# Kernel tuning notes

Hardware: AMD Instinct MI355X
Metric: run time of the kernel (lower is better)

The kernel has to match this reference:

```python
import jax, jax.numpy as jnp
import numpy as np

T, E, H = 65536, 512, 512  # seq_len, embedding_size, hidden_size (kernel_size=2)


def setup_inputs() -> dict:
    key = jax.random.key(0)
    k1, k2 = jax.random.split(key)
    x = jax.random.normal(k1, (T, E), dtype=jnp.float32)
    # nn.Linear(2*E, 3*H): weight [3H, 2E], bias [3H]. Store transposed for x @ W.
    W = jax.random.normal(k2, (2 * E, 3 * H), dtype=jnp.float32) * 0.02
    b = jnp.zeros((3 * H,), dtype=jnp.float32)
    return {"input": x, "W": W, "b": b}


def reference(input, W, b):
    x = input
    t, e = x.shape
    h_dim = W.shape[1] // 3
    # Shift input by one step (zero-padded) and concat: conv over kernel_size=2 window.
    x_prev = jnp.concatenate([jnp.zeros((1, e), x.dtype), x[:-1]], axis=0)  # [T, E]
    gates = jnp.concatenate([x, x_prev], axis=1) @ W + b  # [T, 3H]
    z = jnp.tanh(gates[:, :h_dim])                # cell candidate
    f = jax.nn.sigmoid(gates[:, h_dim:2 * h_dim])  # forget gate
    o = jax.nn.sigmoid(gates[:, 2 * h_dim:])       # output gate

    # fo-pool recurrence: c_t = f_t * c_{t-1} + (1 - f_t) * z_t ; h_t = o_t * c_t
    def step(c, zfo):
        z_t, f_t, o_t = zfo
        c_new = f_t * c + (1.0 - f_t) * z_t
        return c_new, (c_new, o_t * c_new)

    c0 = jnp.zeros((h_dim,), x.dtype)
    _, (cells, hiddens) = jax.lax.scan(step, c0, (z, f, o))
    # Match torch: (hidden_temp [T,H], h [1,H], c [1,H])
    return hiddens, hiddens[-1:], cells[-1:]
```

## Files before the change

kernel.cpp:

```cpp
#include <hip/hip_runtime.h>


#define T_LEN 65536
#define H3    1536
#define LC    64
#define NCHUNK 1024

typedef float f32x4 __attribute__((ext_vector_type(4)));
typedef short bf16x8 __attribute__((ext_vector_type(8)));

__device__ __forceinline__ unsigned short f2bf(float f) {
    unsigned int x = __builtin_bit_cast(unsigned int, f);
    x += 0x7fffu + ((x >> 16) & 1u);
    return (unsigned short)(x >> 16);
}
__device__ __forceinline__ float bf2f(unsigned short u) {
    return __builtin_bit_cast(float, ((unsigned int)u) << 16);
}
__device__ __forceinline__ float fsig(float x)  { return 1.f / (1.f + __expf(-x)); }
__device__ __forceinline__ float ftanh(float x) { return 2.f / (1.f + __expf(-2.f * x)) - 1.f; }

__device__ __forceinline__ void gload_lds16(const void* g, void* l) {
    __builtin_amdgcn_global_load_lds((const __attribute__((address_space(1))) void*)g,
                                     (__attribute__((address_space(3))) void*)l, 16, 0, 0);
}

__global__ void prep_x(const float* __restrict__ x, unsigned short* __restrict__ xp) {
    const long long nq = (512LL + (long long)T_LEN * 512) / 4;
    for (long long q = (long long)blockIdx.x * blockDim.x + threadIdx.x; q < nq;
         q += (long long)gridDim.x * blockDim.x) {
        ushort4 u;
        if (q < 128) {
            u.x = 0; u.y = 0; u.z = 0; u.w = 0;
        } else {
            const float4 v = *reinterpret_cast<const float4*>(x + q * 4 - 512);
            u.x = f2bf(v.x); u.y = f2bf(v.y); u.z = f2bf(v.z); u.w = f2bf(v.w);
        }
        *reinterpret_cast<ushort4*>(xp + q * 4) = u;
    }
}

__global__ void prep_w(const float* __restrict__ W, unsigned short* __restrict__ Wt) {
    const int n_el = 1024 * H3;
    for (int i = blockIdx.x * blockDim.x + threadIdx.x; i < n_el;
         i += gridDim.x * blockDim.x) {
        const int k = i / H3, n = i - k * H3;
        Wt[n * 1024 + k] = f2bf(W[i]);
    }
}

__global__ __launch_bounds__(256) void gemm_gates(
    const unsigned short* __restrict__ xp,
    const unsigned short* __restrict__ Wt,
    const float* __restrict__ bias,
    unsigned short* __restrict__ zfo)
{
    __shared__ unsigned short Alds[2][128 * 32];
    __shared__ unsigned short Blds[2][128 * 32];

    const int tid  = threadIdx.x;
    const int lane = tid & 63;
    const int w    = tid >> 6;
    const int wr   = w >> 1, wc = w & 1;

    const int flat = blockIdx.y * gridDim.x + blockIdx.x;
    const int idx  = (flat & 7) * 768 + (flat >> 3);
    const int nb   = (idx % 12) * 128;
    const long long t0 = (long long)(idx / 12) * 128;

    const int srow_l = lane >> 2;
    const int scol   = (((lane & 3) ^ ((lane >> 3) & 3)) * 8);

    auto stage = [&](int bb, int kt) {
        const int kb = kt * 32;
        const long long abase = (kb < 512) ? (long long)(512 + kb) : (long long)(kb - 512);
        #pragma unroll
        for (int j = 0; j < 2; ++j) {
            const int row = j * 64 + w * 16 + srow_l;
            gload_lds16(xp + abase + (t0 + row) * 512 + scol,
                        &Alds[bb][(j * 64 + w * 16) * 32]);
            gload_lds16(Wt + (long long)(nb + row) * 1024 + kb + scol,
                        &Blds[bb][(j * 64 + w * 16) * 32]);
        }
    };

    const int arow  = lane & 15;
    const int swzco = (((lane >> 4) ^ ((arow >> 1) & 3)) * 8);

    f32x4 acc[4][4] = {};

    stage(0, 0);
    asm volatile("s_waitcnt vmcnt(0)" ::: "memory");
    __syncthreads();

    for (int kt = 0; kt < 32; ++kt) {
        const int bb = kt & 1;
        if (kt + 1 < 32) stage(bb ^ 1, kt + 1);

        bf16x8 af[4], bfr[4];
        #pragma unroll
        for (int m = 0; m < 4; ++m)
            af[m] = *reinterpret_cast<const bf16x8*>(&Alds[bb][(wr * 64 + m * 16 + arow) * 32 + swzco]);
        #pragma unroll
        for (int n = 0; n < 4; ++n)
            bfr[n] = *reinterpret_cast<const bf16x8*>(&Blds[bb][(wc * 64 + n * 16 + arow) * 32 + swzco]);
        #pragma unroll
        for (int m = 0; m < 4; ++m)
            #pragma unroll
            for (int n = 0; n < 4; ++n)
                acc[m][n] = __builtin_amdgcn_mfma_f32_16x16x32_bf16(af[m], bfr[n], acc[m][n], 0, 0, 0);

        if (kt + 1 < 32) { asm volatile("s_waitcnt vmcnt(0)" ::: "memory"); }
        __syncthreads();
    }

    const int cls = nb >> 9;
    float bn[4];
    #pragma unroll
    for (int n = 0; n < 4; ++n) bn[n] = bias[nb + wc * 64 + n * 16 + arow];
    #pragma unroll
    for (int m = 0; m < 4; ++m) {
        #pragma unroll
        for (int n = 0; n < 4; ++n) {
            const int col = nb + wc * 64 + n * 16 + arow;
            #pragma unroll
            for (int j = 0; j < 4; ++j) {
                const long long row = t0 + wr * 64 + m * 16 + (lane >> 4) * 4 + j;
                float v = acc[m][n][j] + bn[n];
                v = (cls == 0) ? ftanh(v) : fsig(v);
                zfo[row * H3 + col] = f2bf(v);
            }
        }
    }
}

__global__ void scan_pass1(const unsigned short* __restrict__ zfo,
                           float* __restrict__ P, float* __restrict__ L) {
    const int chunk = blockIdx.x;
    const int c4    = threadIdx.x;
    const unsigned short* base = zfo + (long long)chunk * LC * H3 + c4 * 4;
    float c[4] = {0.f, 0.f, 0.f, 0.f};
    float p[4] = {1.f, 1.f, 1.f, 1.f};
    for (int t = 0; t < LC; ++t) {
        const unsigned short* row = base + t * H3;
        const ushort4 uz = *reinterpret_cast<const ushort4*>(row);
        const ushort4 uf = *reinterpret_cast<const ushort4*>(row + 512);
        const float z[4] = {bf2f(uz.x), bf2f(uz.y), bf2f(uz.z), bf2f(uz.w)};
        const float f[4] = {bf2f(uf.x), bf2f(uf.y), bf2f(uf.z), bf2f(uf.w)};
        #pragma unroll
        for (int j = 0; j < 4; ++j) {
            c[j] = fmaf(f[j], c[j] - z[j], z[j]);
            p[j] *= f[j];
        }
    }
    #pragma unroll
    for (int j = 0; j < 4; ++j) {
        P[chunk * 512 + c4 * 4 + j] = p[j];
        L[chunk * 512 + c4 * 4 + j] = c[j];
    }
}

__global__ __launch_bounds__(1024) void scan_pass2(
    const float* __restrict__ P, const float* __restrict__ L,
    float* __restrict__ carry, float* __restrict__ out) {
    const int ch = blockIdx.x;
    const int k  = threadIdx.x;
    __shared__ float sP[1024], sL[1024];
    float p = P[k * 512 + ch];
    float l = L[k * 512 + ch];
    sP[k] = p; sL[k] = l;
    __syncthreads();
    for (int d = 1; d < 1024; d <<= 1) {
        float pp = 1.f, ll = 0.f;
        if (k >= d) { pp = sP[k - d]; ll = sL[k - d]; }
        __syncthreads();
        l = fmaf(p, ll, l);
        p = p * pp;
        sP[k] = p; sL[k] = l;
        __syncthreads();
    }
    carry[k * 512 + ch] = (k == 0) ? 0.f : sL[k - 1];
    if (k == 1023) out[(long long)T_LEN * 512 + 512 + ch] = l;
}

__global__ void scan_pass3(const unsigned short* __restrict__ zfo,
                           const float* __restrict__ carry,
                           float* __restrict__ out) {
    const int chunk = blockIdx.x;
    const int c4    = threadIdx.x;
    const unsigned short* base = zfo + (long long)chunk * LC * H3 + c4 * 4;
    float c[4], h[4] = {0.f, 0.f, 0.f, 0.f};
    #pragma unroll
    for (int j = 0; j < 4; ++j) c[j] = carry[chunk * 512 + c4 * 4 + j];
    float4* outp = reinterpret_cast<float4*>(out + (long long)chunk * LC * 512) + c4;
    for (int t = 0; t < LC; ++t) {
        const unsigned short* row = base + t * H3;
        const ushort4 uz = *reinterpret_cast<const ushort4*>(row);
        const ushort4 uf = *reinterpret_cast<const ushort4*>(row + 512);
        const ushort4 uo = *reinterpret_cast<const ushort4*>(row + 1024);
        const float z[4] = {bf2f(uz.x), bf2f(uz.y), bf2f(uz.z), bf2f(uz.w)};
        const float f[4] = {bf2f(uf.x), bf2f(uf.y), bf2f(uf.z), bf2f(uf.w)};
        const float o[4] = {bf2f(uo.x), bf2f(uo.y), bf2f(uo.z), bf2f(uo.w)};
        #pragma unroll
        for (int j = 0; j < 4; ++j) {
            c[j] = fmaf(f[j], c[j] - z[j], z[j]);
            h[j] = o[j] * c[j];
        }
        float4 hv; hv.x = h[0]; hv.y = h[1]; hv.z = h[2]; hv.w = h[3];
        outp[t * 128] = hv;
    }
    if (chunk == NCHUNK - 1) {
        #pragma unroll
        for (int j = 0; j < 4; ++j)
            out[(long long)T_LEN * 512 + c4 * 4 + j] = h[j];
    }
}

extern "C" void kernel_launch(void* const* d_in, const int* in_sizes, int n_in,
                              void* d_out, int out_size, void* d_ws, size_t ws_size,
                              hipStream_t stream) {
    const float* x = (const float*)d_in[0];
    const float* W = (const float*)d_in[1];
    const float* b = (const float*)d_in[2];
    float* out = (float*)d_out;

    char* ws = (char*)d_ws;
    unsigned short* xp  = (unsigned short*)(ws);
    unsigned short* Wt  = (unsigned short*)(ws + 67110912LL);
    unsigned short* zfo = (unsigned short*)(ws + 70256640LL);
    float* P     = (float*)(ws);
    float* L     = (float*)(ws + 4194304LL);
    float* carry = (float*)(ws + 8388608LL);

    prep_x<<<4096, 256, 0, stream>>>(x, xp);
    prep_w<<<768, 256, 0, stream>>>(W, Wt);

    dim3 gg(H3 / 128, T_LEN / 128, 1);
    gemm_gates<<<gg, 256, 0, stream>>>(xp, Wt, b, zfo);

    scan_pass1<<<NCHUNK, 128, 0, stream>>>(zfo, P, L);
    scan_pass2<<<512, 1024, 0, stream>>>(P, L, carry, out);
    scan_pass3<<<NCHUNK, 128, 0, stream>>>(zfo, carry, out);
}
```

Measured before the change: 442.3 us.

## Triple-buffer GEMM LDS staging with partial waitcnt and faster activations

Moves the gates GEMM from double to triple buffering of LDS tiles. Each step waits only for the older loads (vmcnt(4)) and uses a raw s_barrier, so the next tile's global-to-LDS loads overlap the MFMA work. Global pointers are now advanced incrementally, with a jump where the A source switches from the current row to the shifted row. The activations use the hardware exp2 and rcp intrinsics, and launch bounds request 3 blocks per CU. This costs more LDS and risks register or occupancy limits, plus lower accuracy in the approximate sigmoid and tanh.

Result: faster. 393.7 us (-11.0%).

```diff
diff --git a/kernel.cpp b/kernel.cpp
--- a/kernel.cpp
+++ b/kernel.cpp
@@ -17,8 +17,12 @@
 __device__ __forceinline__ float bf2f(unsigned short u) {
     return __builtin_bit_cast(float, ((unsigned int)u) << 16);
 }
-__device__ __forceinline__ float fsig(float x)  { return 1.f / (1.f + __expf(-x)); }
-__device__ __forceinline__ float ftanh(float x) { return 2.f / (1.f + __expf(-2.f * x)) - 1.f; }
+__device__ __forceinline__ float fsig(float x) {
+    return __builtin_amdgcn_rcpf(1.f + __builtin_amdgcn_exp2f(-1.44269504f * x));
+}
+__device__ __forceinline__ float ftanh(float x) {
+    return 2.f * __builtin_amdgcn_rcpf(1.f + __builtin_amdgcn_exp2f(-2.88539008f * x)) - 1.f;
+}
 
 __device__ __forceinline__ void gload_lds16(const void* g, void* l) {
     __builtin_amdgcn_global_load_lds((const __attribute__((address_space(1))) void*)g,
@@ -49,14 +53,14 @@
     }
 }
 
-__global__ __launch_bounds__(256) void gemm_gates(
+__global__ __launch_bounds__(256, 3) void gemm_gates(
     const unsigned short* __restrict__ xp,
     const unsigned short* __restrict__ Wt,
     const float* __restrict__ bias,
     unsigned short* __restrict__ zfo)
 {
-    __shared__ unsigned short Alds[2][128 * 32];
-    __shared__ unsigned short Blds[2][128 * 32];
+    __shared__ unsigned short Alds[3][128 * 32];
+    __shared__ unsigned short Blds[3][128 * 32];
 
     const int tid  = threadIdx.x;
     const int lane = tid & 63;
@@ -71,17 +75,14 @@
     const int srow_l = lane >> 2;
     const int scol   = (((lane & 3) ^ ((lane >> 3) & 3)) * 8);
 
-    auto stage = [&](int bb, int kt) {
-        const int kb = kt * 32;
-        const long long abase = (kb < 512) ? (long long)(512 + kb) : (long long)(kb - 512);
-        #pragma unroll
-        for (int j = 0; j < 2; ++j) {
-            const int row = j * 64 + w * 16 + srow_l;
-            gload_lds16(xp + abase + (t0 + row) * 512 + scol,
-                        &Alds[bb][(j * 64 + w * 16) * 32]);
-            gload_lds16(Wt + (long long)(nb + row) * 1024 + kb + scol,
-                        &Blds[bb][(j * 64 + w * 16) * 32]);
-        }
+    const unsigned short* gA = xp + (t0 + w * 16 + srow_l) * 512 + 512 + scol;
+    const unsigned short* gB = Wt + (long long)(nb + w * 16 + srow_l) * 1024 + scol;
+
+    auto stage = [&](unsigned short* Al, unsigned short* Bl) {
+        gload_lds16(gA,             Al + (w * 16) * 32);
+        gload_lds16(gA + 64 * 512,  Al + ((64 + w * 16)) * 32);
+        gload_lds16(gB,             Bl + (w * 16) * 32);
+        gload_lds16(gB + 64 * 1024, Bl + ((64 + w * 16)) * 32);
     };
 
     const int arow  = lane & 15;
@@ -89,30 +90,53 @@
 
     f32x4 acc[4][4] = {};
 
-    stage(0, 0);
-    asm volatile("s_waitcnt vmcnt(0)" ::: "memory");
-    __syncthreads();
-
-    for (int kt = 0; kt < 32; ++kt) {
-        const int bb = kt & 1;
-        if (kt + 1 < 32) stage(bb ^ 1, kt + 1);
-
+    auto compute = [&](const unsigned short* Al, const unsigned short* Bl) {
         bf16x8 af[4], bfr[4];
         #pragma unroll
         for (int m = 0; m < 4; ++m)
-            af[m] = *reinterpret_cast<const bf16x8*>(&Alds[bb][(wr * 64 + m * 16 + arow) * 32 + swzco]);
+            af[m] = *reinterpret_cast<const bf16x8*>(Al + (wr * 64 + m * 16 + arow) * 32 + swzco);
         #pragma unroll
         for (int n = 0; n < 4; ++n)
-            bfr[n] = *reinterpret_cast<const bf16x8*>(&Blds[bb][(wc * 64 + n * 16 + arow) * 32 + swzco]);
+            bfr[n] = *reinterpret_cast<const bf16x8*>(Bl + (wc * 64 + n * 16 + arow) * 32 + swzco);
         #pragma unroll
         for (int m = 0; m < 4; ++m)
             #pragma unroll
             for (int n = 0; n < 4; ++n)
                 acc[m][n] = __builtin_amdgcn_mfma_f32_16x16x32_bf16(af[m], bfr[n], acc[m][n], 0, 0, 0);
-
-        if (kt + 1 < 32) { asm volatile("s_waitcnt vmcnt(0)" ::: "memory"); }
-        __syncthreads();
-    }
+    };
+
+    stage(Alds[0], Blds[0]); gA += 32; gB += 32;
+    stage(Alds[1], Blds[1]); gA += 32; gB += 32;
+    asm volatile("s_waitcnt vmcnt(4)" ::: "memory");
+    __builtin_amdgcn_s_barrier();
+
+    for (int kt = 0; kt < 30; kt += 3) {
+        {
+            stage(Alds[2], Blds[2]);
+            gA += (kt + 2 == 15) ? -992 : 32;  gB += 32;
+            compute(Alds[0], Blds[0]);
+            asm volatile("s_waitcnt vmcnt(4)" ::: "memory");
+            __builtin_amdgcn_s_barrier();
+        }
+        {
+            stage(Alds[0], Blds[0]);
+            gA += (kt + 3 == 15) ? -992 : 32;  gB += 32;
+            compute(Alds[1], Blds[1]);
+            asm volatile("s_waitcnt vmcnt(4)" ::: "memory");
+            __builtin_amdgcn_s_barrier();
+        }
+        {
+            stage(Alds[1], Blds[1]);
+            gA += (kt + 4 == 15) ? -992 : 32;  gB += 32;
+            compute(Alds[2], Blds[2]);
+            asm volatile("s_waitcnt vmcnt(4)" ::: "memory");
+            __builtin_amdgcn_s_barrier();
+        }
+    }
+    compute(Alds[0], Blds[0]);
+    asm volatile("s_waitcnt vmcnt(0)" ::: "memory");
+    __builtin_amdgcn_s_barrier();
+    compute(Alds[1], Blds[1]);
 
     const int cls = nb >> 9;
     float bn[4];
```

## Rewrite gates GEMM with 256x256 tiles, 8 waves, ping-pong pipelined LDS staging

Applied to the files above, without the earlier changes.

The gates GEMM moves from 128x128 tiles with 4 waves and K-step 32 to 256x256 tiles with 8 waves and K-step 64. The main loop is hand-scheduled into quarter-steps that interleave LDS fragment reads, async global-to-LDS loads and MFMA bursts. It uses partial vmcnt waits, raw barriers and s_setprio around the MFMA groups. The aim is more reuse per loaded byte and better overlap of loads with compute, at the cost of higher register pressure and a 128KB LDS footprint that limits the GPU to one block per CU. The activations are also switched to native exp2 and reciprocal intrinsics.

Result: faster. 402.2 us (-9.1%).

```diff
diff --git a/kernel.cpp b/kernel.cpp
--- a/kernel.cpp
+++ b/kernel.cpp
@@ -17,13 +17,22 @@
 __device__ __forceinline__ float bf2f(unsigned short u) {
     return __builtin_bit_cast(float, ((unsigned int)u) << 16);
 }
-__device__ __forceinline__ float fsig(float x)  { return 1.f / (1.f + __expf(-x)); }
-__device__ __forceinline__ float ftanh(float x) { return 2.f / (1.f + __expf(-2.f * x)) - 1.f; }
+__device__ __forceinline__ float fsig(float x) {
+    return __builtin_amdgcn_rcpf(1.f + __builtin_amdgcn_exp2f(-1.44269504f * x));
+}
+__device__ __forceinline__ float ftanh(float x) {
+    return 2.f * __builtin_amdgcn_rcpf(1.f + __builtin_amdgcn_exp2f(-2.88539008f * x)) - 1.f;
+}
 
 __device__ __forceinline__ void gload_lds16(const void* g, void* l) {
     __builtin_amdgcn_global_load_lds((const __attribute__((address_space(1))) void*)g,
                                      (__attribute__((address_space(3))) void*)l, 16, 0, 0);
 }
+
+#define BARX()  __builtin_amdgcn_s_barrier()
+#define LGKM0() asm volatile("s_waitcnt lgkmcnt(0)" ::: "memory")
+#define VM4()   asm volatile("s_waitcnt vmcnt(4)" ::: "memory")
+#define VM0()   asm volatile("s_waitcnt vmcnt(0)" ::: "memory")
 
 __global__ void prep_x(const float* __restrict__ x, unsigned short* __restrict__ xp) {
     const long long nq = (512LL + (long long)T_LEN * 512) / 4;
@@ -49,86 +58,133 @@
     }
 }
 
-__global__ __launch_bounds__(256) void gemm_gates(
+__global__ __launch_bounds__(512, 1) void gemm_gates(
     const unsigned short* __restrict__ xp,
     const unsigned short* __restrict__ Wt,
     const float* __restrict__ bias,
     unsigned short* __restrict__ zfo)
 {
-    __shared__ unsigned short Alds[2][128 * 32];
-    __shared__ unsigned short Blds[2][128 * 32];
+    __shared__ unsigned short lds[2 * 4 * 8192];
 
     const int tid  = threadIdx.x;
     const int lane = tid & 63;
-    const int w    = tid >> 6;
-    const int wr   = w >> 1, wc = w & 1;
+    const int wid  = tid >> 6;
+    const int wm   = wid >> 2;
+    const int wn   = wid & 3;
 
     const int flat = blockIdx.y * gridDim.x + blockIdx.x;
-    const int idx  = (flat & 7) * 768 + (flat >> 3);
-    const int nb   = (idx % 12) * 128;
-    const long long t0 = (long long)(idx / 12) * 128;
-
-    const int srow_l = lane >> 2;
-    const int scol   = (((lane & 3) ^ ((lane >> 3) & 3)) * 8);
-
-    auto stage = [&](int bb, int kt) {
-        const int kb = kt * 32;
-        const long long abase = (kb < 512) ? (long long)(512 + kb) : (long long)(kb - 512);
+    const int idx  = (flat & 7) * 192 + (flat >> 3);
+    const int nb   = (idx % 6) * 256;
+    const long long t0 = (long long)(idx / 6) * 256;
+
+    const int trow = tid >> 3;
+    const int scol = ((tid & 7) ^ (trow & 7)) * 8;
+
+    auto stA = [&](int b, int h, int kb) {
+        const int abase = (kb < 512) ? (512 + kb) : (kb - 512);
+        const unsigned short* g = xp + (t0 + h * 128 + trow) * 512 + abase + scol;
+        unsigned short* l = (unsigned short*)lds + b * 32768 + h * 8192 + wid * 512;
+        gload_lds16(g, l);
+        gload_lds16(g + 64 * 512, l + 4096);
+    };
+    auto stB = [&](int b, int h, int kb) {
+        const unsigned short* g = Wt + (long long)(nb + h * 128 + trow) * 1024 + kb + scol;
+        unsigned short* l = (unsigned short*)lds + b * 32768 + (2 + h) * 8192 + wid * 512;
+        gload_lds16(g, l);
+        gload_lds16(g + 64 * 1024, l + 4096);
+    };
+
+    const int arow = lane & 15;
+    const int q4   = lane >> 4;
+    const int sA0  = ((q4)     ^ (arow & 7)) * 8;
+    const int sA1  = ((q4 + 4) ^ (arow & 7)) * 8;
+    const unsigned short* Ab = (const unsigned short*)lds + wm * 8192 + arow * 64;
+    const unsigned short* Bb = (const unsigned short*)lds + (2 + (wn >> 1)) * 8192
+                               + ((wn & 1) * 64 + arow) * 64;
+
+    f32x4  acc[8][4] = {};
+    bf16x8 a[4][2];
+    bf16x8 b[4][2];
+
+    #define RD_A4(bo, mbase)                                                     \
+        _Pragma("unroll")                                                        \
+        for (int m = 0; m < 4; ++m) {                                            \
+            a[m][0] = *(const bf16x8*)(Ab + (bo) + ((mbase) + m) * 1024 + sA0);  \
+            a[m][1] = *(const bf16x8*)(Ab + (bo) + ((mbase) + m) * 1024 + sA1);  \
+        }
+    #define RD_B2(bo, n0)                                                        \
+        _Pragma("unroll")                                                        \
+        for (int n = 0; n < 2; ++n) {                                            \
+            b[(n0)+n][0] = *(const bf16x8*)(Bb + (bo) + ((n0)+n) * 1024 + sA0);  \
+            b[(n0)+n][1] = *(const bf16x8*)(Bb + (bo) + ((n0)+n) * 1024 + sA1);  \
+        }
+    #define QUAD(mh, nh)                                                         \
+        __builtin_amdgcn_s_setprio(1);                                           \
+        _Pragma("unroll")                                                        \
+        for (int n = 0; n < 2; ++n) {                                            \
+            _Pragma("unroll")                                                    \
+            for (int m = 0; m < 4; ++m) {                                        \
+                acc[(mh)*4+m][(nh)*2+n] = __builtin_amdgcn_mfma_f32_16x16x32_bf16( \
+                    a[m][0], b[(nh)*2+n][0], acc[(mh)*4+m][(nh)*2+n], 0, 0, 0);  \
+                acc[(mh)*4+m][(nh)*2+n] = __builtin_amdgcn_mfma_f32_16x16x32_bf16( \
+                    a[m][1], b[(nh)*2+n][1], acc[(mh)*4+m][(nh)*2+n], 0, 0, 0);  \
+            }                                                                    \
+        }                                                                        \
+        __builtin_amdgcn_s_setprio(0);
+
+    stB(0, 0, 0); stA(0, 0, 0); stA(0, 1, 0); stB(0, 1, 0);
+    stB(1, 0, 64); stA(1, 0, 64);
+    VM4();
+    BARX();
+
+    for (int i = 0; i < 7; ++i) {
+        const int kb1 = i * 128 + 64;
+        const int kb2 = i * 128 + 128;
+        const int kb3 = i * 128 + 192;
+        { RD_A4(0, 0); RD_B2(0, 0); RD_B2(0, 2); stA(1, 1, kb1);
+          BARX(); LGKM0(); QUAD(0, 0); BARX(); }
+        { stB(1, 1, kb1);
+          BARX(); LGKM0(); QUAD(0, 1); BARX(); }
+        { RD_A4(0, 4); stB(0, 0, kb2);
+          BARX(); LGKM0(); QUAD(1, 0); BARX(); }
+        { stA(0, 0, kb2);
+          BARX(); LGKM0(); QUAD(1, 1); VM4(); BARX(); }
+        { RD_A4(32768, 0); RD_B2(32768, 0); RD_B2(32768, 2); stA(0, 1, kb2);
+          BARX(); LGKM0(); QUAD(0, 0); BARX(); }
+        { stB(0, 1, kb2);
+          BARX(); LGKM0(); QUAD(0, 1); BARX(); }
+        { RD_A4(32768, 4); stB(1, 0, kb3);
+          BARX(); LGKM0(); QUAD(1, 0); BARX(); }
+        { stA(1, 0, kb3);
+          BARX(); LGKM0(); QUAD(1, 1); VM4(); BARX(); }
+    }
+    { RD_A4(0, 0); RD_B2(0, 0); RD_B2(0, 2); stA(1, 1, 960);
+      BARX(); LGKM0(); QUAD(0, 0); BARX(); }
+    { stB(1, 1, 960);
+      BARX(); LGKM0(); QUAD(0, 1); BARX(); }
+    { RD_A4(0, 4);
+      BARX(); LGKM0(); QUAD(1, 0); BARX(); }
+    { BARX(); LGKM0(); QUAD(1, 1); VM0(); BARX(); }
+    { RD_A4(32768, 0); RD_B2(32768, 0); RD_B2(32768, 2);
+      BARX(); LGKM0(); QUAD(0, 0); BARX(); }
+    { BARX(); LGKM0(); QUAD(0, 1); BARX(); }
+    { RD_A4(32768, 4);
+      BARX(); LGKM0(); QUAD(1, 0); BARX(); }
+    { LGKM0(); QUAD(1, 1); }
+
+    const int cls = nb >> 9;
+    #pragma unroll
+    for (int n = 0; n < 4; ++n) {
+        const int col = nb + wn * 64 + n * 16 + arow;
+        const float bn_ = bias[col];
         #pragma unroll
-        for (int j = 0; j < 2; ++j) {
-            const int row = j * 64 + w * 16 + srow_l;
-            gload_lds16(xp + abase + (t0 + row) * 512 + scol,
-                        &Alds[bb][(j * 64 + w * 16) * 32]);
-            gload_lds16(Wt + (long long)(nb + row) * 1024 + kb + scol,
-                        &Blds[bb][(j * 64 + w * 16) * 32]);
-        }
-    };
-
-    const int arow  = lane & 15;
-    const int swzco = (((lane >> 4) ^ ((arow >> 1) & 3)) * 8);
-
-    f32x4 acc[4][4] = {};
-
-    stage(0, 0);
-    asm volatile("s_waitcnt vmcnt(0)" ::: "memory");
-    __syncthreads();
-
-    for (int kt = 0; kt < 32; ++kt) {
-        const int bb = kt & 1;
-        if (kt + 1 < 32) stage(bb ^ 1, kt + 1);
-
-        bf16x8 af[4], bfr[4];
-        #pragma unroll
-        for (int m = 0; m < 4; ++m)
-            af[m] = *reinterpret_cast<const bf16x8*>(&Alds[bb][(wr * 64 + m * 16 + arow) * 32 + swzco]);
-        #pragma unroll
-        for (int n = 0; n < 4; ++n)
-            bfr[n] = *reinterpret_cast<const bf16x8*>(&Blds[bb][(wc * 64 + n * 16 + arow) * 32 + swzco]);
-        #pragma unroll
-        for (int m = 0; m < 4; ++m)
-            #pragma unroll
-            for (int n = 0; n < 4; ++n)
-                acc[m][n] = __builtin_amdgcn_mfma_f32_16x16x32_bf16(af[m], bfr[n], acc[m][n], 0, 0, 0);
-
-        if (kt + 1 < 32) { asm volatile("s_waitcnt vmcnt(0)" ::: "memory"); }
-        __syncthreads();
-    }
-
-    const int cls = nb >> 9;
-    float bn[4];
-    #pragma unroll
-    for (int n = 0; n < 4; ++n) bn[n] = bias[nb + wc * 64 + n * 16 + arow];
-    #pragma unroll
-    for (int m = 0; m < 4; ++m) {
-        #pragma unroll
-        for (int n = 0; n < 4; ++n) {
-            const int col = nb + wc * 64 + n * 16 + arow;
+        for (int m = 0; m < 8; ++m) {
+            const long long row0 = t0 + wm * 128 + m * 16 + q4 * 4;
             #pragma unroll
             for (int j = 0; j < 4; ++j) {
-                const long long row = t0 + wr * 64 + m * 16 + (lane >> 4) * 4 + j;
-                float v = acc[m][n][j] + bn[n];
+                float v = acc[m][n][j] + bn_;
                 v = (cls == 0) ? ftanh(v) : fsig(v);
-                zfo[row * H3 + col] = f2bf(v);
+                zfo[(row0 + j) * H3 + col] = f2bf(v);
             }
         }
     }
@@ -235,8 +291,8 @@
     prep_x<<<4096, 256, 0, stream>>>(x, xp);
     prep_w<<<768, 256, 0, stream>>>(W, Wt);
 
-    dim3 gg(H3 / 128, T_LEN / 128, 1);
-    gemm_gates<<<gg, 256, 0, stream>>>(xp, Wt, b, zfo);
+    dim3 gg(H3 / 256, T_LEN / 256, 1);
+    gemm_gates<<<gg, 512, 0, stream>>>(xp, Wt, b, zfo);
 
     scan_pass1<<<NCHUNK, 128, 0, stream>>>(zfo, P, L);
     scan_pass2<<<512, 1024, 0, stream>>>(P, L, carry, out);
```
